# Kernel optimization log

Hardware: AMD Instinct MI355X
Metric: run time of the kernel (lower is better)

Reference implementation:

```python
import jax, jax.numpy as jnp
import numpy as np

THETA = 100000.0

def _rope(x, pos, theta=THETA):
    # x: [..., H, S, d_k]; pos: [S] int
    d_k = x.shape[-1]
    half = d_k // 2
    inv_freq = theta ** (-(jnp.arange(half, dtype=jnp.float32) / half))  # theta^{-2i/d}
    ang = pos.astype(jnp.float32)[:, None] * inv_freq[None, :]  # [S, half]
    cos, sin = jnp.cos(ang), jnp.sin(ang)
    x1 = x[..., 0::2]
    x2 = x[..., 1::2]
    r1 = x1 * cos - x2 * sin
    r2 = x1 * sin + x2 * cos
    # interleave back to [..., d_k]
    return jnp.stack([r1, r2], axis=-1).reshape(x.shape)


def setup_inputs() -> dict:
    key = jax.random.key(0)
    ks = jax.random.split(key, 5)
    B, S, D = 1, 4096, 1024
    x = jax.random.normal(ks[0], (B, S, D), dtype=jnp.float32)
    sc = 1.0 / np.sqrt(D)
    Wq = jax.random.normal(ks[1], (D, D), dtype=jnp.float32) * sc
    Wk = jax.random.normal(ks[2], (D, D), dtype=jnp.float32) * sc
    Wv = jax.random.normal(ks[3], (D, D), dtype=jnp.float32) * sc
    Wo = jax.random.normal(ks[4], (D, D), dtype=jnp.float32) * sc
    token_positions = jnp.arange(S, dtype=jnp.int32)
    return {"x": x, "Wq": Wq, "Wk": Wk, "Wv": Wv, "Wo": Wo, "token_positions": token_positions}


def reference(x, Wq, Wk, Wv, Wo, token_positions):
    H = 16
    B, S, D = x.shape
    d_k = D // H
    # Linear (no bias): y = x @ W^T
    Q = jnp.einsum('bsd,ed->bse', x, Wq)
    K = jnp.einsum('bsd,ed->bse', x, Wk)
    V = jnp.einsum('bsd,ed->bse', x, Wv)
    # [B, H, S, d_k]
    Q = Q.reshape(B, S, H, d_k).transpose(0, 2, 1, 3)
    K = K.reshape(B, S, H, d_k).transpose(0, 2, 1, 3)
    V = V.reshape(B, S, H, d_k).transpose(0, 2, 1, 3)
    Q = _rope(Q, token_positions)
    K = _rope(K, token_positions)
    scores = jnp.einsum('bhqd,bhkd->bhqk', Q, K) / jnp.sqrt(jnp.float32(d_k))
    causal = jnp.tril(jnp.ones((S, S), dtype=bool))
    scores = jnp.where(causal, scores, jnp.finfo(scores.dtype).min)
    probs = jax.nn.softmax(scores, axis=-1)
    attn = jnp.einsum('bhqk,bhkd->bhqd', probs, V)
    attn = attn.transpose(0, 2, 1, 3).reshape(B, S, D)
    return jnp.einsum('bsd,ed->bse', attn, Wo)
```

## Files before the change

### kernel.cpp

```cpp
#include <hip/hip_runtime.h>

typedef float f32x4 __attribute__((ext_vector_type(4)));
typedef short s16x8 __attribute__((ext_vector_type(8)));
typedef int   i32x2 __attribute__((ext_vector_type(2)));
typedef int   i32x4 __attribute__((ext_vector_type(4)));

#define DEV static __device__ __forceinline__

DEV short f2bf(float f) {
    unsigned u = __builtin_bit_cast(unsigned, f);
    u += 0x7FFFu + ((u >> 16) & 1u);
    return (short)(u >> 16);
}
DEV float bf2f(short s) {
    return __builtin_bit_cast(float, ((unsigned)(unsigned short)s) << 16);
}
DEV int cvtpk(float lo, float hi) {
    int r;
    asm("v_cvt_pk_bf16_f32 %0, %1, %2" : "=v"(r) : "v"(lo), "v"(hi));
    return r;
}
DEV float fexp2(float x) { float r; asm("v_exp_f32 %0, %1" : "=v"(r) : "v"(x)); return r; }
DEV float ffract(float x){ float r; asm("v_fract_f32 %0, %1" : "=v"(r) : "v"(x)); return r; }
DEV float fsin(float x)  { float r; asm("v_sin_f32 %0, %1" : "=v"(r) : "v"(x)); return r; }
DEV float fcos(float x)  { float r; asm("v_cos_f32 %0, %1" : "=v"(r) : "v"(x)); return r; }
DEV f32x4 mfma_bf16(s16x8 a, s16x8 b, f32x4 c) {
    asm("v_mfma_f32_16x16x32_bf16 %0, %1, %2, %0" : "+v"(c) : "v"(a), "v"(b));
    return c;
}
DEV f32x4 mfma16_bf16(i32x2 a, i32x2 b, f32x4 c) {
    asm("v_mfma_f32_16x16x16_bf16 %0, %1, %2, %0" : "+v"(c) : "v"(a), "v"(b));
    return c;
}
DEV void gl_lds16(const void* g, void* l) {
    __builtin_amdgcn_global_load_lds((const __attribute__((address_space(1))) unsigned*)g,
                                     (__attribute__((address_space(3))) unsigned*)l, 16, 0, 0);
}

__global__ __launch_bounds__(256) void conv_kernel(
    const float* __restrict__ x,
    const float* __restrict__ W0, const float* __restrict__ W1,
    const float* __restrict__ W2, const float* __restrict__ W3,
    short* __restrict__ xb,
    short* __restrict__ B0, short* __restrict__ B1,
    short* __restrict__ B2, short* __restrict__ B3)
{
    const int bid = blockIdx.x, tid = threadIdx.x;
    const float* src;
    short* dst;
    size_t off;
    if (bid < 2048) {
        src = x; dst = xb; off = (size_t)bid * 2048 + tid * 8;
    } else {
        int t = bid - 2048, wi = t >> 9;
        src = wi == 0 ? W0 : (wi == 1 ? W1 : (wi == 2 ? W2 : W3));
        dst = wi == 0 ? B0 : (wi == 1 ? B1 : (wi == 2 ? B2 : B3));
        off = (size_t)(t & 511) * 2048 + tid * 8;
    }
    f32x4 v0 = *(const f32x4*)(src + off);
    f32x4 v1 = *(const f32x4*)(src + off + 4);
    s16x8 o;
    #pragma unroll
    for (int e = 0; e < 4; e++) { o[e] = f2bf(v0[e]); o[4 + e] = f2bf(v1[e]); }
    *(s16x8*)(dst + off) = o;
}

template<int BM, int OUT_BF16, int ROPE>
__global__ __launch_bounds__(256) void gemm128(
    const short* __restrict__ A,
    const short* __restrict__ Bq, const short* __restrict__ Bk, const short* __restrict__ Bv,
    void* __restrict__ Cq, void* __restrict__ Ck, void* __restrict__ Cv,
    const int* __restrict__ posp)
{
    constexpr int KD = 1024, ND = 1024;
    constexpr int MI = BM / 32;
    __shared__ __align__(16) short As[BM * 32];
    __shared__ __align__(16) short Bs[128 * 32];
    const int n0 = blockIdx.x * 128, m0 = blockIdx.y * BM;
    const int zz = blockIdx.z;
    const short* B = zz == 0 ? Bq : (zz == 1 ? Bk : Bv);
    void* C       = zz == 0 ? Cq : (zz == 1 ? Ck : Cv);
    const int tid = threadIdx.x;
    const int lane = tid & 63, w = tid >> 6, g = lane >> 4, c = lane & 15;
    const int wm = w >> 1, wn = w & 1;

    const int swz = (tid & 3) ^ ((tid >> 3) & 3);
    const short* a0 = A + (size_t)(m0 + (tid >> 2)) * KD + 8 * swz;
    const short* a1 = a0 + (size_t)64 * KD;
    const short* b0 = B + (size_t)(n0 + (tid >> 2)) * KD + 8 * swz;
    const short* b1 = b0 + (size_t)64 * KD;
    char* ldsA = (char*)As + w * 1024;
    char* ldsB = (char*)Bs + w * 1024;

    int aoff[MI], boff[4];
    #pragma unroll
    for (int i = 0; i < MI; i++) {
        int ar = wm * (BM / 2) + i * 16 + c;
        aoff[i] = ar * 64 + (g ^ ((ar >> 1) & 3)) * 16;
    }
    #pragma unroll
    for (int j = 0; j < 4; j++) {
        int br = wn * 64 + j * 16 + c;
        boff[j] = br * 64 + (g ^ ((br >> 1) & 3)) * 16;
    }

    f32x4 acc[MI][4] = {};

    for (int k0 = 0; k0 < KD; k0 += 32) {
        __syncthreads();
        gl_lds16(a0 + k0, ldsA);
        if (BM == 128) gl_lds16(a1 + k0, ldsA + 4096);
        gl_lds16(b0 + k0, ldsB);
        gl_lds16(b1 + k0, ldsB + 4096);
        __syncthreads();
        s16x8 af[MI], bf[4];
        #pragma unroll
        for (int i = 0; i < MI; i++) af[i] = *(const s16x8*)((const char*)As + aoff[i]);
        #pragma unroll
        for (int j = 0; j < 4; j++) bf[j] = *(const s16x8*)((const char*)Bs + boff[j]);
        #pragma unroll
        for (int i = 0; i < MI; i++)
            #pragma unroll
            for (int j = 0; j < 4; j++)
                acc[i][j] = mfma_bf16(af[i], bf[j], acc[i][j]);
    }

    if (ROPE && zz <= 1) {
        const float ps = (zz == 0) ? 0.18033688011112042f : 1.0f;
        #pragma unroll
        for (int j = 0; j < 4; j++) {
            int col = n0 + wn * 64 + j * 16 + c;
            float invf = fexp2(-(float)((col & 63) >> 1) * 0.51905126482615036f)
                       * 0.15915494309189535f;
            float ssign = (col & 1) ? 1.f : -1.f;
            #pragma unroll
            for (int i = 0; i < MI; i++)
                #pragma unroll
                for (int r = 0; r < 4; r++) {
                    int row = m0 + wm * (BM / 2) + i * 16 + 4 * g + r;
                    float fp = (float)posp[row];
                    float fr = ffract(fp * invf);
                    float sn = fsin(fr) * ps, cs = fcos(fr) * ps;
                    float own = acc[i][j][r];
                    float oth = __shfl_xor(own, 1);
                    acc[i][j][r] = own * cs + oth * (ssign * sn);
                }
        }
    }

    #pragma unroll
    for (int i = 0; i < MI; i++)
        #pragma unroll
        for (int j = 0; j < 4; j++)
            #pragma unroll
            for (int r = 0; r < 4; r++) {
                int row = m0 + wm * (BM / 2) + i * 16 + 4 * g + r;
                int col = n0 + wn * 64 + j * 16 + c;
                float v = acc[i][j][r];
                if (OUT_BF16) ((short*)C)[(size_t)row * ND + col] = f2bf(v);
                else          ((float*)C)[(size_t)row * ND + col] = v;
            }
}

template<int A_BF16, int OUT_BF16>
__global__ __launch_bounds__(256) void gemm_bt(
    const void* __restrict__ Ap,
    const float* __restrict__ B0, const float* __restrict__ B1, const float* __restrict__ B2,
    void* __restrict__ C0, void* __restrict__ C1, void* __restrict__ C2)
{
    constexpr int KD = 1024, ND = 1024;
    __shared__ short As[64][40];
    __shared__ short Bs[64][40];
    const int n0 = blockIdx.x * 64, m0 = blockIdx.y * 64;
    const float* Bw = blockIdx.z == 0 ? B0 : (blockIdx.z == 1 ? B1 : B2);
    void* Cw       = blockIdx.z == 0 ? C0 : (blockIdx.z == 1 ? C1 : C2);
    const int tid = threadIdx.x;
    const int lane = tid & 63, w = tid >> 6, g = lane >> 4, c = lane & 15;
    const int wm = w >> 1, wn = w & 1;
    const int sr = tid >> 2, scc = (tid & 3) * 8;

    f32x4 acc[2][2] = {};

    for (int k0 = 0; k0 < KD; k0 += 32) {
        __syncthreads();
        if (A_BF16) {
            *(s16x8*)&As[sr][scc] =
                *(const s16x8*)((const short*)Ap + (size_t)(m0 + sr) * KD + k0 + scc);
        } else {
            const float* ap = (const float*)Ap + (size_t)(m0 + sr) * KD + k0 + scc;
            f32x4 va = *(const f32x4*)ap, vb = *(const f32x4*)(ap + 4);
            s16x8 av;
            #pragma unroll
            for (int e = 0; e < 4; e++) { av[e] = f2bf(va[e]); av[4 + e] = f2bf(vb[e]); }
            *(s16x8*)&As[sr][scc] = av;
        }
        {
            const float* bp = Bw + (size_t)(n0 + sr) * KD + k0 + scc;
            f32x4 va = *(const f32x4*)bp, vb = *(const f32x4*)(bp + 4);
            s16x8 bv;
            #pragma unroll
            for (int e = 0; e < 4; e++) { bv[e] = f2bf(va[e]); bv[4 + e] = f2bf(vb[e]); }
            *(s16x8*)&Bs[sr][scc] = bv;
        }
        __syncthreads();
        s16x8 af[2], bfv[2];
        #pragma unroll
        for (int i = 0; i < 2; i++) af[i]  = *(const s16x8*)&As[wm * 32 + i * 16 + c][8 * g];
        #pragma unroll
        for (int j = 0; j < 2; j++) bfv[j] = *(const s16x8*)&Bs[wn * 32 + j * 16 + c][8 * g];
        #pragma unroll
        for (int i = 0; i < 2; i++)
            #pragma unroll
            for (int j = 0; j < 2; j++)
                acc[i][j] = mfma_bf16(af[i], bfv[j], acc[i][j]);
    }

    #pragma unroll
    for (int i = 0; i < 2; i++)
        #pragma unroll
        for (int j = 0; j < 2; j++)
            #pragma unroll
            for (int r = 0; r < 4; r++) {
                int row = m0 + wm * 32 + i * 16 + 4 * g + r;
                int col = n0 + wn * 32 + j * 16 + c;
                float v = acc[i][j][r];
                if (OUT_BF16) ((short*)Cw)[(size_t)row * ND + col] = f2bf(v);
                else          ((float*)Cw)[(size_t)row * ND + col] = v;
            }
}

__global__ __launch_bounds__(256) void rope_kernel(short* Q, short* K, const int* __restrict__ posp)
{
    const int t = blockIdx.x * 256 + threadIdx.x;
    const int isK = blockIdx.y;
    short* ptr = isK ? K : Q;
    const float postscale = isK ? 1.0f : 0.18033688011112042f;
    const int idx  = t * 8;
    const int srow = idx >> 10;
    const int dd   = (idx & 1023) & 63;
    const int p0   = dd >> 1;
    const float fp = (float)posp[srow];
    s16x8 v = *(s16x8*)(ptr + idx);
    s16x8 o;
    #pragma unroll
    for (int pr = 0; pr < 4; pr++) {
        float ex  = fexp2(-(float)(p0 + pr) * 0.51905126482615036f);
        float ang = fp * ex * 0.15915494309189535f;
        float fr  = ffract(ang);
        float sn  = fsin(fr) * postscale;
        float cs  = fcos(fr) * postscale;
        float x1 = bf2f(v[2 * pr]), x2 = bf2f(v[2 * pr + 1]);
        o[2 * pr]     = f2bf(x1 * cs - x2 * sn);
        o[2 * pr + 1] = f2bf(x1 * sn + x2 * cs);
    }
    *(s16x8*)(ptr + idx) = o;
}

template<int SPLIT>
__global__ __launch_bounds__(256, 5) void attn_kernel(
    const short* __restrict__ Q, const short* __restrict__ K,
    const short* __restrict__ V, short* __restrict__ O0,
    short* __restrict__ O1, float* __restrict__ Lf)
{
    constexpr int D = 1024;
    constexpr int ST = 1 + SPLIT;
    int bx, h, z;
    if (SPLIT) {
        const int B = blockIdx.x;
        const int xcd = B & 7, k = B >> 3;
        h = xcd + 8 * (k >> 6);
        const int r = k & 63;
        bx = r & 31;
        z = r >> 5;
    } else {
        bx = blockIdx.x; h = blockIdx.y; z = 0;
    }
    const int hc = h * 64;
    short* O = (SPLIT && z) ? O1 : O0;
    const int tid = threadIdx.x;
    const int w = tid >> 6, lane = tid & 63, g = lane >> 4, c = lane & 15;

    __shared__ __align__(16) int Kl[2][64 * 32];
    __shared__ __align__(16) int Vl[2][64][32];

    const int krow_l = lane >> 3;
    const int kchunk = (lane & 7) ^ krow_l;
    const short* Kpre = K + hc + (size_t)(w * 16 + krow_l) * D + kchunk * 8;
    char* kdst0 = (char*)&Kl[0][0] + w * 16 * 128;
    char* kdst1 = (char*)&Kl[1][0] + w * 16 * 128;

    const int vkvp = tid & 31;
    const int vd0 = (tid >> 5) * 8;
    const short* Vpre = V + hc + (size_t)(2 * vkvp) * D + vd0;

    int koff0[4], koff1[4];
    #pragma unroll
    for (int t = 0; t < 4; t++) {
        int row = t * 16 + c;
        koff0[t] = row * 128 + ((g) ^ (row & 7)) * 16;
        koff1[t] = row * 128 + ((4 + g) ^ (row & 7)) * 16;
    }

    for (int pi = 0; pi < 2; pi++) {
        const int qb = pi ? 63 - bx : bx;
        const int qrow = qb * 64 + w * 16 + c;
        const short* qp = Q + (size_t)qrow * D + hc + 8 * g;
        const s16x8 bq0 = *(const s16x8*)qp;
        const s16x8 bq1 = *(const s16x8*)(qp + 32);

        f32x4 acc[4] = {};
        float l = 0.f;
        const int nkb = qb + 1;

        __syncthreads();
        s16x8 vs0, vs1;
        if (z < nkb) {
            gl_lds16(Kpre + (size_t)(z * 64) * D, kdst0);
            gl_lds16(Kpre + (size_t)(z * 64 + 8) * D, kdst0 + 8 * 128);
            const short* vp = Vpre + (size_t)(z * 64) * D;
            vs0 = *(const s16x8*)vp;
            vs1 = *(const s16x8*)(vp + D);
        }

        int cur = 0;
        for (int kb = z; kb < nkb; kb += ST, cur ^= 1) {
            #pragma unroll
            for (int e = 0; e < 8; e++) {
                unsigned dw = (unsigned)(unsigned short)vs0[e] | ((unsigned)(unsigned short)vs1[e] << 16);
                Vl[cur][vd0 + e][vkvp ^ (4 * e)] = (int)dw;
            }
            asm volatile("s_waitcnt vmcnt(0)" ::: "memory");
            __syncthreads();

            const bool more = (kb + ST) < nkb;
            if (more) {
                const int kb1 = kb + ST;
                char* kd = cur ? kdst0 : kdst1;
                gl_lds16(Kpre + (size_t)(kb1 * 64) * D, kd);
                gl_lds16(Kpre + (size_t)(kb1 * 64 + 8) * D, kd + 8 * 128);
                const short* vp = Vpre + (size_t)(kb1 * 64) * D;
                vs0 = *(const s16x8*)vp;
                vs1 = *(const s16x8*)(vp + D);
            }

            const char* Kb = (const char*)&Kl[cur][0];
            f32x4 st[4];
            __builtin_amdgcn_s_setprio(1);
            #pragma unroll
            for (int t = 0; t < 4; t++) {
                s16x8 a0 = *(const s16x8*)(Kb + koff0[t]);
                s16x8 a1 = *(const s16x8*)(Kb + koff1[t]);
                f32x4 zf = {};
                zf = mfma_bf16(a0, bq0, zf);
                zf = mfma_bf16(a1, bq1, zf);
                st[t] = zf;
            }
            __builtin_amdgcn_s_setprio(0);

            float p[16];
            if (kb == qb) {
                #pragma unroll
                for (int t = 0; t < 4; t++)
                    #pragma unroll
                    for (int i = 0; i < 4; i++) {
                        int kv = kb * 64 + t * 16 + 4 * g + i;
                        float e = fexp2(st[t][i]);
                        if (kv > qrow) e = 0.f;
                        p[t * 4 + i] = e;
                        l += e;
                    }
            } else {
                #pragma unroll
                for (int t = 0; t < 4; t++)
                    #pragma unroll
                    for (int i = 0; i < 4; i++) {
                        float e = fexp2(st[t][i]);
                        p[t * 4 + i] = e;
                        l += e;
                    }
            }

            i32x2 pd[4];
            #pragma unroll
            for (int t = 0; t < 4; t++) {
                pd[t][0] = cvtpk(p[t * 4 + 0], p[t * 4 + 1]);
                pd[t][1] = cvtpk(p[t * 4 + 2], p[t * 4 + 3]);
            }

            __builtin_amdgcn_s_setprio(1);
            #pragma unroll
            for (int t = 0; t < 4; t++) {
                #pragma unroll
                for (int jt = 0; jt < 4; jt++) {
                    i32x2 vb = *(const i32x2*)&Vl[cur][jt * 16 + c][(t * 8 + 2 * g) ^ (4 * (c & 7))];
                    acc[jt] = mfma16_bf16(pd[t], vb, acc[jt]);
                }
            }
            __builtin_amdgcn_s_setprio(0);
        }

        float lsum = l + __shfl_xor(l, 16);
        lsum += __shfl_xor(lsum, 32);
        if (SPLIT && lane < 16) {
            float Lv = (lsum > 0.f) ? __log2f(lsum) : -1e30f;
            Lf[(size_t)(z * 16 + h) * 4096 + (qb * 64 + w * 16 + lane)] = Lv;
        }
        float linv[4];
        #pragma unroll
        for (int i = 0; i < 4; i++) {
            float ls = __shfl(lsum, 4 * g + i);
            linv[i] = (ls > 0.f) ? 1.f / ls : 0.f;
        }
        #pragma unroll
        for (int jt = 0; jt < 4; jt++)
            #pragma unroll
            for (int i = 0; i < 4; i++) {
                int r = qb * 64 + w * 16 + 4 * g + i;
                O[(size_t)r * D + hc + jt * 16 + c] = f2bf(acc[jt][i] * linv[i]);
            }
    }
}

__global__ __launch_bounds__(256) void combine_kernel(
    short* __restrict__ Aw, const short* __restrict__ P1, const float* __restrict__ Lf)
{
    const int t = blockIdx.x * 256 + threadIdx.x;
    const int idx = t * 8;
    const int row = idx >> 10, col = idx & 1023, h = col >> 6;
    float L0 = Lf[(size_t)h * 4096 + row];
    float L1 = Lf[(size_t)(16 + h) * 4096 + row];
    float LM = fmaxf(L0, L1);
    float w0 = fexp2(L0 - LM), w1 = fexp2(L1 - LM);
    float inv = 1.f / (w0 + w1);
    w0 *= inv; w1 *= inv;
    s16x8 a = *(s16x8*)(Aw + idx);
    s16x8 b = *(const s16x8*)(P1 + idx);
    s16x8 o;
    #pragma unroll
    for (int e = 0; e < 8; e++)
        o[e] = f2bf(w0 * bf2f(a[e]) + w1 * bf2f(b[e]));
    *(s16x8*)(Aw + idx) = o;
}

extern "C" void kernel_launch(void* const* d_in, const int* in_sizes, int n_in,
                              void* d_out, int out_size, void* d_ws, size_t ws_size,
                              hipStream_t stream)
{
    const float* x  = (const float*)d_in[0];
    const float* Wq = (const float*)d_in[1];
    const float* Wk = (const float*)d_in[2];
    const float* Wv = (const float*)d_in[3];
    const float* Wo = (const float*)d_in[4];
    const int*  pos = (const int*)d_in[5];
    float* out = (float*)d_out;

    const size_t SD = (size_t)4096 * 1024;
    const size_t WSZ = (size_t)1024 * 1024;
    short* Qw = (short*)d_ws;
    short* Kw = Qw + SD;
    short* Vw = Kw + SD;
    short* Aw = Vw + SD;

    const size_t need_A = (5 * SD + 4 * WSZ) * sizeof(short) + 2 * 16 * 4096 * sizeof(float);
    const size_t need_B = (4 * SD + 4 * WSZ) * sizeof(short);

    if (ws_size >= need_A) {
        short* P1  = Aw + SD;
        short* xb  = Aw;
        short* Wqb = P1 + SD;
        short* Wkb = Wqb + WSZ;
        short* Wvb = Wkb + WSZ;
        short* Wob = Wvb + WSZ;
        float* Lf  = (float*)(Wob + WSZ);
        conv_kernel<<<4096, 256, 0, stream>>>(x, Wq, Wk, Wv, Wo, xb, Wqb, Wkb, Wvb, Wob);
        gemm128<128, 1, 1><<<dim3(8, 32, 3), 256, 0, stream>>>(xb, Wqb, Wkb, Wvb, Qw, Kw, Vw, pos);
        attn_kernel<1><<<1024, 256, 0, stream>>>(Qw, Kw, Vw, Aw, P1, Lf);
        combine_kernel<<<2048, 256, 0, stream>>>(Aw, P1, Lf);
        gemm128<64, 0, 0><<<dim3(8, 64, 1), 256, 0, stream>>>(Aw, Wob, Wob, Wob, out, out, out, pos);
    } else if (ws_size >= need_B) {
        short* xb  = Aw;
        short* Wqb = Aw + SD;
        short* Wkb = Wqb + WSZ;
        short* Wvb = Wkb + WSZ;
        short* Wob = Wvb + WSZ;
        conv_kernel<<<4096, 256, 0, stream>>>(x, Wq, Wk, Wv, Wo, xb, Wqb, Wkb, Wvb, Wob);
        gemm128<128, 1, 1><<<dim3(8, 32, 3), 256, 0, stream>>>(xb, Wqb, Wkb, Wvb, Qw, Kw, Vw, pos);
        attn_kernel<0><<<dim3(32, 16, 1), 256, 0, stream>>>(Qw, Kw, Vw, Aw, Aw, nullptr);
        gemm128<64, 0, 0><<<dim3(8, 64, 1), 256, 0, stream>>>(Aw, Wob, Wob, Wob, out, out, out, pos);
    } else {
        gemm_bt<0, 1><<<dim3(16, 64, 3), 256, 0, stream>>>(x, Wq, Wk, Wv, Qw, Kw, Vw);
        rope_kernel<<<dim3(2048, 2), 256, 0, stream>>>(Qw, Kw, pos);
        attn_kernel<0><<<dim3(32, 16, 1), 256, 0, stream>>>(Qw, Kw, Vw, Aw, Aw, nullptr);
        gemm_bt<1, 0><<<dim3(16, 64, 1), 256, 0, stream>>>(Aw, Wo, Wo, Wo, out, out, out);
    }
}
```

Baseline: 139.0 us.

## Use 512-thread attention blocks covering 128 query rows with warp-specialized K/V loads

The attention kernel now runs 8 waves per block over a 128-row query tile, so each K/V tile staged in LDS is shared by twice as many query rows. Waves 0-3 issue the async K loads and waves 4-7 load and transpose V, splitting the load work by wave role. Waves whose rows lie entirely above the current key block skip the compute, and the causal mask is applied whenever the block overlaps the diagonal. Grid sizes are halved to match, which lowers the block count and occupancy per CU and adds some idle waves near the diagonal.

```diff
diff --git a/kernel.cpp b/kernel.cpp
--- a/kernel.cpp
+++ b/kernel.cpp
@@ -257,23 +257,23 @@
 }
 
 template<int SPLIT>
-__global__ __launch_bounds__(256, 5) void attn_kernel(
+__global__ __launch_bounds__(512, 2) void attn_kernel(
     const short* __restrict__ Q, const short* __restrict__ K,
     const short* __restrict__ V, short* __restrict__ O0,
     short* __restrict__ O1, float* __restrict__ Lf)
 {
     constexpr int D = 1024;
     constexpr int ST = 1 + SPLIT;
-    int bx, h, z;
+    int qx, h, z;
     if (SPLIT) {
         const int B = blockIdx.x;
         const int xcd = B & 7, k = B >> 3;
-        h = xcd + 8 * (k >> 6);
-        const int r = k & 63;
-        bx = r & 31;
-        z = r >> 5;
+        h = xcd + 8 * (k >> 5);
+        const int r = k & 31;
+        qx = r & 15;
+        z = r >> 4;
     } else {
-        bx = blockIdx.x; h = blockIdx.y; z = 0;
+        qx = blockIdx.x; h = blockIdx.y; z = 0;
     }
     const int hc = h * 64;
     short* O = (SPLIT && z) ? O1 : O0;
@@ -283,14 +283,16 @@
     __shared__ __align__(16) int Kl[2][64 * 32];
     __shared__ __align__(16) int Vl[2][64][32];
 
+    const int wk = w & 3;
     const int krow_l = lane >> 3;
     const int kchunk = (lane & 7) ^ krow_l;
-    const short* Kpre = K + hc + (size_t)(w * 16 + krow_l) * D + kchunk * 8;
-    char* kdst0 = (char*)&Kl[0][0] + w * 16 * 128;
-    char* kdst1 = (char*)&Kl[1][0] + w * 16 * 128;
-
-    const int vkvp = tid & 31;
-    const int vd0 = (tid >> 5) * 8;
+    const short* Kpre = K + hc + (size_t)(wk * 16 + krow_l) * D + kchunk * 8;
+    char* kdst0 = (char*)&Kl[0][0] + wk * 16 * 128;
+    char* kdst1 = (char*)&Kl[1][0] + wk * 16 * 128;
+
+    const int vtid = tid & 255;
+    const int vkvp = vtid & 31;
+    const int vd0 = (vtid >> 5) * 8;
     const short* Vpre = V + hc + (size_t)(2 * vkvp) * D + vd0;
 
     int koff0[4], koff1[4];
@@ -302,32 +304,38 @@
     }
 
     for (int pi = 0; pi < 2; pi++) {
-        const int qb = pi ? 63 - bx : bx;
-        const int qrow = qb * 64 + w * 16 + c;
+        const int qq = pi ? 31 - qx : qx;
+        const int wq_min = qq * 128 + w * 16;
+        const int qrow = wq_min + c;
         const short* qp = Q + (size_t)qrow * D + hc + 8 * g;
         const s16x8 bq0 = *(const s16x8*)qp;
         const s16x8 bq1 = *(const s16x8*)(qp + 32);
 
         f32x4 acc[4] = {};
         float l = 0.f;
-        const int nkb = qb + 1;
+        const int nkb = 2 * qq + 2;
 
         __syncthreads();
         s16x8 vs0, vs1;
-        if (z < nkb) {
-            gl_lds16(Kpre + (size_t)(z * 64) * D, kdst0);
-            gl_lds16(Kpre + (size_t)(z * 64 + 8) * D, kdst0 + 8 * 128);
-            const short* vp = Vpre + (size_t)(z * 64) * D;
-            vs0 = *(const s16x8*)vp;
-            vs1 = *(const s16x8*)(vp + D);
+        {
+            if (w < 4) {
+                gl_lds16(Kpre + (size_t)(z * 64) * D, kdst0);
+                gl_lds16(Kpre + (size_t)(z * 64 + 8) * D, kdst0 + 8 * 128);
+            } else {
+                const short* vp = Vpre + (size_t)(z * 64) * D;
+                vs0 = *(const s16x8*)vp;
+                vs1 = *(const s16x8*)(vp + D);
+            }
         }
 
         int cur = 0;
         for (int kb = z; kb < nkb; kb += ST, cur ^= 1) {
-            #pragma unroll
-            for (int e = 0; e < 8; e++) {
-                unsigned dw = (unsigned)(unsigned short)vs0[e] | ((unsigned)(unsigned short)vs1[e] << 16);
-                Vl[cur][vd0 + e][vkvp ^ (4 * e)] = (int)dw;
+            if (w >= 4) {
+                #pragma unroll
+                for (int e = 0; e < 8; e++) {
+                    unsigned dw = (unsigned)(unsigned short)vs0[e] | ((unsigned)(unsigned short)vs1[e] << 16);
+                    Vl[cur][vd0 + e][vkvp ^ (4 * e)] = (int)dw;
+                }
             }
             asm volatile("s_waitcnt vmcnt(0)" ::: "memory");
             __syncthreads();
@@ -335,13 +343,18 @@
             const bool more = (kb + ST) < nkb;
             if (more) {
                 const int kb1 = kb + ST;
-                char* kd = cur ? kdst0 : kdst1;
-                gl_lds16(Kpre + (size_t)(kb1 * 64) * D, kd);
-                gl_lds16(Kpre + (size_t)(kb1 * 64 + 8) * D, kd + 8 * 128);
-                const short* vp = Vpre + (size_t)(kb1 * 64) * D;
-                vs0 = *(const s16x8*)vp;
-                vs1 = *(const s16x8*)(vp + D);
-            }
+                if (w < 4) {
+                    char* kd = cur ? kdst0 : kdst1;
+                    gl_lds16(Kpre + (size_t)(kb1 * 64) * D, kd);
+                    gl_lds16(Kpre + (size_t)(kb1 * 64 + 8) * D, kd + 8 * 128);
+                } else {
+                    const short* vp = Vpre + (size_t)(kb1 * 64) * D;
+                    vs0 = *(const s16x8*)vp;
+                    vs1 = *(const s16x8*)(vp + D);
+                }
+            }
+
+            if (kb * 64 > wq_min + 15) continue;
 
             const char* Kb = (const char*)&Kl[cur][0];
             f32x4 st[4];
@@ -358,7 +371,7 @@
             __builtin_amdgcn_s_setprio(0);
 
             float p[16];
-            if (kb == qb) {
+            if (kb * 64 + 63 > wq_min) {
                 #pragma unroll
                 for (int t = 0; t < 4; t++)
                     #pragma unroll
@@ -403,7 +416,7 @@
         lsum += __shfl_xor(lsum, 32);
         if (SPLIT && lane < 16) {
             float Lv = (lsum > 0.f) ? __log2f(lsum) : -1e30f;
-            Lf[(size_t)(z * 16 + h) * 4096 + (qb * 64 + w * 16 + lane)] = Lv;
+            Lf[(size_t)(z * 16 + h) * 4096 + (qq * 128 + w * 16 + lane)] = Lv;
         }
         float linv[4];
         #pragma unroll
@@ -415,7 +428,7 @@
         for (int jt = 0; jt < 4; jt++)
             #pragma unroll
             for (int i = 0; i < 4; i++) {
-                int r = qb * 64 + w * 16 + 4 * g + i;
+                int r = qq * 128 + w * 16 + 4 * g + i;
                 O[(size_t)r * D + hc + jt * 16 + c] = f2bf(acc[jt][i] * linv[i]);
             }
     }
@@ -474,7 +487,7 @@
         float* Lf  = (float*)(Wob + WSZ);
         conv_kernel<<<4096, 256, 0, stream>>>(x, Wq, Wk, Wv, Wo, xb, Wqb, Wkb, Wvb, Wob);
         gemm128<128, 1, 1><<<dim3(8, 32, 3), 256, 0, stream>>>(xb, Wqb, Wkb, Wvb, Qw, Kw, Vw, pos);
-        attn_kernel<1><<<1024, 256, 0, stream>>>(Qw, Kw, Vw, Aw, P1, Lf);
+        attn_kernel<1><<<512, 512, 0, stream>>>(Qw, Kw, Vw, Aw, P1, Lf);
         combine_kernel<<<2048, 256, 0, stream>>>(Aw, P1, Lf);
         gemm128<64, 0, 0><<<dim3(8, 64, 1), 256, 0, stream>>>(Aw, Wob, Wob, Wob, out, out, out, pos);
     } else if (ws_size >= need_B) {
@@ -485,12 +498,12 @@
         short* Wob = Wvb + WSZ;
         conv_kernel<<<4096, 256, 0, stream>>>(x, Wq, Wk, Wv, Wo, xb, Wqb, Wkb, Wvb, Wob);
         gemm128<128, 1, 1><<<dim3(8, 32, 3), 256, 0, stream>>>(xb, Wqb, Wkb, Wvb, Qw, Kw, Vw, pos);
-        attn_kernel<0><<<dim3(32, 16, 1), 256, 0, stream>>>(Qw, Kw, Vw, Aw, Aw, nullptr);
+        attn_kernel<0><<<dim3(16, 16, 1), 512, 0, stream>>>(Qw, Kw, Vw, Aw, Aw, nullptr);
         gemm128<64, 0, 0><<<dim3(8, 64, 1), 256, 0, stream>>>(Aw, Wob, Wob, Wob, out, out, out, pos);
     } else {
         gemm_bt<0, 1><<<dim3(16, 64, 3), 256, 0, stream>>>(x, Wq, Wk, Wv, Qw, Kw, Vw);
         rope_kernel<<<dim3(2048, 2), 256, 0, stream>>>(Qw, Kw, pos);
-        attn_kernel<0><<<dim3(32, 16, 1), 256, 0, stream>>>(Qw, Kw, Vw, Aw, Aw, nullptr);
+        attn_kernel<0><<<dim3(16, 16, 1), 512, 0, stream>>>(Qw, Kw, Vw, Aw, Aw, nullptr);
         gemm_bt<1, 0><<<dim3(16, 64, 1), 256, 0, stream>>>(Aw, Wo, Wo, Wo, out, out, out);
     }
 }
```

Measured after the change: 131.2 us (median of 2 runs). 5.6% less time.
